# Optimization experiments

Hardware: AMD Instinct MI355X
Metric: run time of the kernel (lower is better)

The kernel has to match this reference:

```python
import jax, jax.numpy as jnp
import numpy as np

EPS = 1e-8
SAMPLE = 4          # minimal_sample_size for homography
BATCH = 1024        # batch_size: hypotheses per iteration
MAX_ITER = 10       # max_iter
MAX_LO = 5          # max_lo_iters
INL_TH = 2.0        # inl_th (on squared transfer error, as in kornia)
CONF = 0.99         # confidence
SOFT_INL_TH = 3.0   # kornia find_homography_dlt_iterated default
DLT_ITERS = 5       # kornia iterated-DLT default n_iter
N_PTS = 4096


def to_homog(p):
    return jnp.concatenate([p, jnp.ones_like(p[..., :1])], axis=-1)


def transform_points(T, p):
    # T: (B,3,3), p: (B,N,2)
    out = jnp.einsum('bij,bnj->bni', T, to_homog(p))
    z = out[..., 2:3]
    zi = jnp.where(jnp.abs(z) > EPS, 1.0 / z, 1.0)
    return out[..., :2] * zi


def normalize_points(p):
    # Hartley normalization: zero mean, mean distance sqrt(2)
    mean = p.mean(axis=1, keepdims=True)                       # (B,1,2)
    scale = jnp.linalg.norm(p - mean, axis=-1).mean(axis=-1)    # (B,)
    s = jnp.asarray(np.sqrt(2.0), p.dtype) / (scale + EPS)
    z = jnp.zeros_like(s)
    o = jnp.ones_like(s)
    T = jnp.stack([s, z, -s * mean[:, 0, 0],
                   z, s, -s * mean[:, 0, 1],
                   z, z, o], axis=-1).reshape(-1, 3, 3)
    return transform_points(T, p), T


def find_homography_dlt(p1, p2, w):
    # p1, p2: (B,N,2); w: (B,N) -> (B,3,3)
    p1n, T1 = normalize_points(p1)
    p2n, T2 = normalize_points(p2)
    x1, y1 = p1n[..., 0], p1n[..., 1]
    x2, y2 = p2n[..., 0], p2n[..., 1]
    o = jnp.ones_like(x1)
    z = jnp.zeros_like(x1)
    ax = jnp.stack([z, z, z, -x1, -y1, -o, y2 * x1, y2 * y1, y2], axis=-1)
    ay = jnp.stack([x1, y1, o, z, z, z, -x2 * x1, -x2 * y1, -x2], axis=-1)
    A = jnp.concatenate([ax, ay], axis=1)           # (B,2N,9); row order irrelevant for A^T W A
    wr = jnp.concatenate([w, w], axis=1)            # weight paired to each row
    AtWA = jnp.einsum('bni,bn,bnj->bij', A, wr, A)  # (B,9,9) symmetric PSD
    _, evecs = jnp.linalg.eigh(AtWA)
    H = evecs[..., :, 0].reshape(-1, 3, 3)          # smallest eigenvector == last right-singular vec
    H = jnp.linalg.inv(T2) @ H @ T1
    return H / (H[..., 2:3, 2:3] + EPS)


def oneway_transfer_error(kp1, kp2, models, squared=True):
    # kp1, kp2: (N,2); models: (B,3,3) -> (B,N)
    out = jnp.einsum('bij,nj->bni', models, to_homog(kp1))
    z = out[..., 2:3]
    zi = jnp.where(jnp.abs(z) > EPS, 1.0 / z, 1.0)
    proj = out[..., :2] * zi
    err = jnp.sum((proj - kp2[None]) ** 2, axis=-1)
    return err if squared else jnp.sqrt(err + EPS)


def find_homography_dlt_iterated(p1, p2, w):
    # iteratively reweighted DLT; mask keeps zero-weight (outlier) rows at zero,
    # equivalent to kornia's hard selection of inlier rows before polishing
    mask = (w > 0).astype(w.dtype)
    H = find_homography_dlt(p1, p2, w)
    for _ in range(DLT_ITERS - 1):
        err = oneway_transfer_error(p1[0], p2[0], H, squared=False)
        w = mask * jnp.exp(-err / (2.0 * SOFT_INL_TH ** 2))
        H = find_homography_dlt(p1, p2, w)
    return H


def sample_is_valid_for_homography(p1, p2):
    # orientation consistency of all point triplets (sign of triple product)
    idx = jnp.array([[0, 1, 2], [0, 1, 3], [0, 2, 3], [1, 2, 3]])
    s1 = jnp.sign(jnp.linalg.det(to_homog(p1)[:, idx]))
    s2 = jnp.sign(jnp.linalg.det(to_homog(p2)[:, idx]))
    return jnp.all(s1 == s2, axis=1)


def ransac_forward(kp1, kp2):
    N = kp1.shape[0]
    dtype = kp1.dtype
    keys = jax.random.split(jax.random.key(42), MAX_ITER)

    def verify(models):
        err = oneway_transfer_error(kp1, kp2, models)
        inl = err <= INL_TH
        return inl, inl.astype(dtype).sum(axis=1)

    def polish_step(carry, _):
        model, inliers, score, active = carry
        w = inliers.astype(dtype)[None]
        model_lo = find_homography_dlt_iterated(kp1[None], kp2[None], w)
        inl_lo, score_lo = verify(model_lo)
        better = active & (score_lo[0] > score)  # 'break' on first non-improvement
        model = jnp.where(better, model_lo[0], model)
        inliers = jnp.where(better, inl_lo[0], inliers)
        score = jnp.where(better, score_lo[0], score)
        return (model, inliers, score, better), None

    def step(carry, xs):
        best_model, best_inl, best_score, done = carry
        key, i = xs
        # minimal sampler: topk over uniform noise == random 4-subset per hypothesis
        rand = jax.random.uniform(key, (BATCH, N), dtype)
        _, idxs = jax.lax.top_k(rand, SAMPLE)
        k1s, k2s = kp1[idxs], kp2[idxs]              # (BATCH,4,2)
        valid = sample_is_valid_for_homography(k1s, k2s)
        models = find_homography_dlt(k1s, k2s, jnp.ones((BATCH, SAMPLE), dtype))
        diag_ok = jnp.abs(jnp.diagonal(models, axis1=1, axis2=2)).min(axis=1) > 1e-4
        inl_all, scores = verify(models)
        scores = jnp.where(valid & diag_ok, scores, -1.0)  # masking == removal for argmax
        bi = jnp.argmax(scores)
        model, inliers, score = models[bi], inl_all[bi], scores[bi]
        improve = (~done) & (score > best_score)
        (model_p, inl_p, score_p, _), _ = jax.lax.scan(
            polish_step, (model, inliers, score, improve), None, length=MAX_LO)
        best_model = jnp.where(improve, model_p, best_model)
        best_inl = jnp.where(improve, inl_p, best_inl)
        best_score = jnp.where(improve, score_p, best_score)
        # early stopping criterion (device-side instead of host .item())
        ratio = jnp.floor(best_score) / N
        q = jnp.clip(1.0 - ratio ** SAMPLE, 1e-12, 1.0 - 1e-12)
        max_samp = jnp.where(best_score >= N, 1.0,
                             jnp.log(1.0 - CONF) / jnp.log(q))
        done = done | (improve & (((i + 1) * BATCH) >= jnp.floor(max_samp)))
        return (best_model, best_inl, best_score, done), None

    init = (jnp.zeros((3, 3), dtype), jnp.zeros((N,), bool),
            jnp.asarray(float(SAMPLE), dtype), jnp.asarray(False))
    (best_model, best_inl, _, _), _ = jax.lax.scan(
        step, init, (keys, jnp.arange(MAX_ITER)))
    return best_model, best_inl


def setup_inputs() -> dict:
    key = jax.random.key(0)
    k1, k2, k3, k4 = jax.random.split(key, 4)
    kp1 = jax.random.uniform(k1, (N_PTS, 2), jnp.float32) * 1024.0
    Ht = jnp.array([[0.9, 0.1, 20.0], [-0.05, 1.05, -10.0], [1e-4, -1e-4, 1.0]], jnp.float32)
    ph = to_homog(kp1) @ Ht.T
    p2 = ph[:, :2] / ph[:, 2:3]
    noise = jax.random.normal(k2, (N_PTS, 2), jnp.float32) * 0.3
    outliers = jax.random.uniform(k3, (N_PTS, 2), jnp.float32) * 1024.0
    is_out = jax.random.uniform(k4, (N_PTS, 1)) < 0.3
    kp2 = jnp.where(is_out, outliers, p2 + noise)
    return {"kp1": kp1, "kp2": kp2}


def reference(kp1, kp2):
    return ransac_forward(kp1, kp2)
```

## Files before the change

kernel.cpp:

```cpp
#include <hip/hip_runtime.h>
#include <cstdint>

#define NPTS   4096
#define NBATCH 1024
#define NIT    10

__host__ __device__ inline uint32_t rotl32(uint32_t v, uint32_t r){ return (v<<r)|(v>>(32u-r)); }

__host__ __device__ inline void tf2x32(uint32_t k0,uint32_t k1,uint32_t x0,uint32_t x1,
                                       uint32_t&o0,uint32_t&o1){
  uint32_t ks2 = k0 ^ k1 ^ 0x1BD11BDAu;
  x0 += k0; x1 += k1;
  x0+=x1; x1=rotl32(x1,13); x1^=x0;
  x0+=x1; x1=rotl32(x1,15); x1^=x0;
  x0+=x1; x1=rotl32(x1,26); x1^=x0;
  x0+=x1; x1=rotl32(x1, 6); x1^=x0;
  x0+=k1; x1+=ks2+1u;
  x0+=x1; x1=rotl32(x1,17); x1^=x0;
  x0+=x1; x1=rotl32(x1,29); x1^=x0;
  x0+=x1; x1=rotl32(x1,16); x1^=x0;
  x0+=x1; x1=rotl32(x1,24); x1^=x0;
  x0+=ks2; x1+=k0+2u;
  x0+=x1; x1=rotl32(x1,13); x1^=x0;
  x0+=x1; x1=rotl32(x1,15); x1^=x0;
  x0+=x1; x1=rotl32(x1,26); x1^=x0;
  x0+=x1; x1=rotl32(x1, 6); x1^=x0;
  x0+=k0; x1+=k1+3u;
  x0+=x1; x1=rotl32(x1,17); x1^=x0;
  x0+=x1; x1=rotl32(x1,29); x1^=x0;
  x0+=x1; x1=rotl32(x1,16); x1^=x0;
  x0+=x1; x1=rotl32(x1,24); x1^=x0;
  x0+=k1; x1+=ks2+4u;
  x0+=x1; x1=rotl32(x1,13); x1^=x0;
  x0+=x1; x1=rotl32(x1,15); x1^=x0;
  x0+=x1; x1=rotl32(x1,26); x1^=x0;
  x0+=x1; x1=rotl32(x1, 6); x1^=x0;
  x0+=ks2; x1+=k0+5u;
  o0=x0; o1=x1;
}

__device__ inline float errsq_f(const float H[9], float x, float y, float kx, float ky){
  float z  = H[6]*x + H[7]*y + H[8];
  float zi = (fabsf(z) > 1e-8f) ? (1.0f/z) : 1.0f;
  float px = (H[0]*x + H[1]*y + H[2])*zi;
  float py = (H[3]*x + H[4]*y + H[5])*zi;
  float dx = px - kx, dy = py - ky;
  return dx*dx + dy*dy;
}

__device__ inline void denorm_h(const double h[9], double s1, double m1x, double m1y,
                                double s2, double m2x, double m2y, float out[9]){
  double G[3][3];
  #pragma unroll
  for(int r=0;r<3;r++){
    double h0=h[3*r], h1=h[3*r+1], h2=h[3*r+2];
    G[r][0] = h0*s1;
    G[r][1] = h1*s1;
    G[r][2] = -s1*m1x*h0 - s1*m1y*h1 + h2;
  }
  double Hm[3][3];
  double inv2 = 1.0/s2;
  #pragma unroll
  for(int c=0;c<3;c++){
    Hm[0][c] = G[0][c]*inv2 + m2x*G[2][c];
    Hm[1][c] = G[1][c]*inv2 + m2y*G[2][c];
    Hm[2][c] = G[2][c];
  }
  double invd = 1.0/(Hm[2][2] + 1e-8);
  #pragma unroll
  for(int r=0;r<3;r++)
    #pragma unroll
    for(int c=0;c<3;c++)
      out[3*r+c] = (float)(Hm[r][c]*invd);
}

__device__ inline double det3c(double ax,double ay, double bx,double by, double cx,double cy){
  return ax*(by-cy) - bx*(ay-cy) + cx*(ay-by);
}

__device__ inline void h4pt(const double P[4][2], double M[3][3]){
  double c0 = det3c(P[3][0],P[3][1], P[1][0],P[1][1], P[2][0],P[2][1]);
  double c1 = det3c(P[0][0],P[0][1], P[3][0],P[3][1], P[2][0],P[2][1]);
  double c2 = det3c(P[0][0],P[0][1], P[1][0],P[1][1], P[3][0],P[3][1]);
  M[0][0]=c0*P[0][0]; M[0][1]=c1*P[1][0]; M[0][2]=c2*P[2][0];
  M[1][0]=c0*P[0][1]; M[1][1]=c1*P[1][1]; M[1][2]=c2*P[2][1];
  M[2][0]=c0;         M[2][1]=c1;         M[2][2]=c2;
}

__device__ inline void adj3(const double M[3][3], double A[3][3]){
  A[0][0]=M[1][1]*M[2][2]-M[1][2]*M[2][1];
  A[0][1]=M[0][2]*M[2][1]-M[0][1]*M[2][2];
  A[0][2]=M[0][1]*M[1][2]-M[0][2]*M[1][1];
  A[1][0]=M[1][2]*M[2][0]-M[1][0]*M[2][2];
  A[1][1]=M[0][0]*M[2][2]-M[0][2]*M[2][0];
  A[1][2]=M[0][2]*M[1][0]-M[0][0]*M[1][2];
  A[2][0]=M[1][0]*M[2][1]-M[1][1]*M[2][0];
  A[2][1]=M[0][1]*M[2][0]-M[0][0]*M[2][1];
  A[2][2]=M[0][0]*M[1][1]-M[0][1]*M[1][0];
}

__device__ inline void ins4(uint64_t b[4], uint64_t k){
  if(k > b[0]){ b[3]=b[2]; b[2]=b[1]; b[1]=b[0]; b[0]=k; }
  else if(k > b[1]){ b[3]=b[2]; b[2]=b[1]; b[1]=k; }
  else if(k > b[2]){ b[3]=b[2]; b[2]=k; }
  else if(k > b[3]){ b[3]=k; }
}

__device__ inline void inv3sym(const double A[3][3], double R[3][3]){
  double a=A[0][0], b=A[1][0], c=A[2][0], d=A[1][1], e=A[2][1], f=A[2][2];
  double C00=d*f-e*e, C01=c*e-b*f, C02=b*e-c*d;
  double det=a*C00+b*C01+c*C02;
  if(det < 1e-300) det = 1e-300;
  double id=1.0/det;
  R[0][0]=C00*id; R[0][1]=C01*id; R[0][2]=C02*id;
  R[1][0]=C01*id; R[1][1]=(a*f-c*c)*id; R[1][2]=(b*c-a*e)*id;
  R[2][0]=C02*id; R[2][1]=R[1][2];      R[2][2]=(a*d-b*b)*id;
}
__device__ inline void mv3(const double M[3][3], const double x[3], double y[3]){
  y[0]=M[0][0]*x[0]+M[0][1]*x[1]+M[0][2]*x[2];
  y[1]=M[1][0]*x[0]+M[1][1]*x[1]+M[1][2]*x[2];
  y[2]=M[2][0]*x[0]+M[2][1]*x[1]+M[2][2]*x[2];
}

__device__ inline void solve24x(const double* sMd, float curHn[9], float curH[9],
                                bool dnorm, double ns1,double nm1x,double nm1y,
                                double ns2,double nm2x,double nm2y){
  double S0[3][3],S1[3][3],S2[3][3],S3[3][3];
  auto unpackd=[&](const double* s, double M[3][3]){
    M[0][0]=s[0]; M[0][1]=s[1]; M[0][2]=s[3];
    M[1][0]=s[1]; M[1][1]=s[2]; M[1][2]=s[4];
    M[2][0]=s[3]; M[2][1]=s[4]; M[2][2]=s[5];
  };
  unpackd(sMd+0,S0); unpackd(sMd+6,S1); unpackd(sMd+12,S2); unpackd(sMd+18,S3);

  double S0i[3][3]; inv3sym(S0,S0i);
  double T1[3][3], T2[3][3];
  #pragma unroll
  for(int i=0;i<3;i++)
    #pragma unroll
    for(int j=0;j<3;j++){
      T1[i][j]=S0i[i][0]*S1[0][j]+S0i[i][1]*S1[1][j]+S0i[i][2]*S1[2][j];
      T2[i][j]=S0i[i][0]*S2[0][j]+S0i[i][1]*S2[1][j]+S0i[i][2]*S2[2][j];
    }
  double Sc[3][3];
  #pragma unroll
  for(int i=0;i<3;i++)
    #pragma unroll
    for(int j=0;j<3;j++){
      double s = S3[i][j];
      #pragma unroll
      for(int k=0;k<3;k++) s -= S1[i][k]*T1[k][j] + S2[i][k]*T2[k][j];
      Sc[i][j]=s;
    }
  double Sci[3][3]; inv3sym(Sc,Sci);

  double v[9];
  #pragma unroll
  for(int i=0;i<9;i++) v[i]=1.0;
  #pragma unroll
  for(int itn=0; itn<2; itn++){
    double a[3]={v[0],v[1],v[2]}, b[3]={v[3],v[4],v[5]}, c[3]={v[6],v[7],v[8]};
    double w1[3],w2[3];
    mv3(S0i,a,w1); mv3(S0i,b,w2);
    double rhs[3];
    #pragma unroll
    for(int j=0;j<3;j++)
      rhs[j] = c[j] + T1[0][j]*a[0]+T1[1][j]*a[1]+T1[2][j]*a[2]
                    + T2[0][j]*b[0]+T2[1][j]*b[1]+T2[2][j]*b[2];
    double rr[3];
    mv3(Sci,rhs,rr);
    #pragma unroll
    for(int i=0;i<3;i++){
      v[i]   = w1[i] + T1[i][0]*rr[0]+T1[i][1]*rr[1]+T1[i][2]*rr[2];
      v[3+i] = w2[i] + T2[i][0]*rr[0]+T2[i][1]*rr[1]+T2[i][2]*rr[2];
      v[6+i] = rr[i];
    }
    if(itn==0){
      double mx=0.0;
      #pragma unroll
      for(int i=0;i<9;i++){ double aa=fabs(v[i]); if(aa>mx) mx=aa; }
      double sc = 1.0/(mx + 1e-300);
      #pragma unroll
      for(int i=0;i<9;i++) v[i]*=sc;
    }
  }
  double n2=0.0;
  #pragma unroll
  for(int i=0;i<9;i++) n2 += v[i]*v[i];
  double invn = 1.0/sqrt(n2);
  #pragma unroll
  for(int i=0;i<9;i++) v[i]*=invn;
  #pragma unroll
  for(int j=0;j<9;j++) curHn[j]=(float)v[j];
  if(dnorm) denorm_h(v, ns1,nm1x,nm1y, ns2,nm2x,nm2y, curH);
}

__device__ inline void model4(const double P1[4][2], const double P2[4][2],
                              float Hf[9], int* flag){
  const int TRI[4][3] = {{0,1,2},{0,1,3},{0,2,3},{1,2,3}};
  bool valid = true;
  #pragma unroll
  for(int tq=0;tq<4;tq++){
    const int i0=TRI[tq][0], i1=TRI[tq][1], i2=TRI[tq][2];
    double d1 = det3c(P1[i0][0],P1[i0][1], P1[i1][0],P1[i1][1], P1[i2][0],P1[i2][1]);
    double d2 = det3c(P2[i0][0],P2[i0][1], P2[i1][0],P2[i1][1], P2[i2][0],P2[i2][1]);
    int s1 = (d1>0.0)-(d1<0.0), s2 = (d2>0.0)-(d2<0.0);
    if(s1 != s2) valid = false;
  }
  double MA[3][3], MB[3][3], AJ[3][3], H[3][3];
  h4pt(P1, MA); h4pt(P2, MB);
  adj3(MA, AJ);
  #pragma unroll
  for(int i=0;i<3;i++)
    #pragma unroll
    for(int j=0;j<3;j++)
      H[i][j] = MB[i][0]*AJ[0][j] + MB[i][1]*AJ[1][j] + MB[i][2]*AJ[2][j];
  double n2=0.0;
  #pragma unroll
  for(int i=0;i<3;i++)
    #pragma unroll
    for(int j=0;j<3;j++) n2 += H[i][j]*H[i][j];
  double invn = 1.0/sqrt(n2);
  double invd = 1.0/(H[2][2]*invn + 1e-8);
  #pragma unroll
  for(int i=0;i<3;i++)
    #pragma unroll
    for(int j=0;j<3;j++) Hf[3*i+j] = (float)(H[i][j]*invn*invd);
  bool diag_ok = (fminf(fminf(fabsf(Hf[0]),fabsf(Hf[4])),fabsf(Hf[8])) > 1e-4f);
  *flag = (valid && diag_ok) ? 1 : 0;
}

__global__ __launch_bounds__(1024) void k_init(const float* __restrict__ kp1,
                                               const float* __restrict__ kp2,
                                               float* stateF, float* nrm,
                                               float* best_inl, float* p1n, float* p2n){
  __shared__ double red[1024];
  const int t = threadIdx.x;
  auto blk_reduce = [&](double v)->double{
    red[t]=v; __syncthreads();
    for(int off=512; off>=1; off>>=1){ if(t<off) red[t]+=red[t+off]; __syncthreads(); }
    double rr = red[0]; __syncthreads(); return rr;
  };
  double sx1=0, sy1=0, sx2=0, sy2=0;
  #pragma unroll
  for(int q=0;q<4;q++){
    int p = t + 1024*q;
    sx1 += (double)kp1[2*p];   sy1 += (double)kp1[2*p+1];
    sx2 += (double)kp2[2*p];   sy2 += (double)kp2[2*p+1];
  }
  double m1x = blk_reduce(sx1)/(double)NPTS;
  double m1y = blk_reduce(sy1)/(double)NPTS;
  double m2x = blk_reduce(sx2)/(double)NPTS;
  double m2y = blk_reduce(sy2)/(double)NPTS;
  double a1=0, a2=0;
  #pragma unroll
  for(int q=0;q<4;q++){
    int p = t + 1024*q;
    double dx1=(double)kp1[2*p]-m1x, dy1=(double)kp1[2*p+1]-m1y;
    double dx2=(double)kp2[2*p]-m2x, dy2=(double)kp2[2*p+1]-m2y;
    a1 += sqrt(dx1*dx1+dy1*dy1);
    a2 += sqrt(dx2*dx2+dy2*dy2);
  }
  double sc1 = blk_reduce(a1)/(double)NPTS;
  double sc2 = blk_reduce(a2)/(double)NPTS;
  double s1 = 1.4142135623730951/(sc1+1e-8);
  double s2 = 1.4142135623730951/(sc2+1e-8);
  if(t==0){
    nrm[0]=(float)s1; nrm[1]=(float)m1x; nrm[2]=(float)m1y;
    nrm[3]=(float)s2; nrm[4]=(float)m2x; nrm[5]=(float)m2y;
    stateF[0]=4.0f; stateF[1]=0.0f;
    for(int j=0;j<9;j++) stateF[2+j]=0.0f;
  }
  #pragma unroll
  for(int q=0;q<4;q++){
    int p = t + 1024*q;
    p1n[2*p]   = (float)(s1*((double)kp1[2*p]  -m1x));
    p1n[2*p+1] = (float)(s1*((double)kp1[2*p+1]-m1y));
    p2n[2*p]   = (float)(s2*((double)kp2[2*p]  -m2x));
    p2n[2*p+1] = (float)(s2*((double)kp2[2*p+1]-m2y));
    best_inl[p] = 0.0f;
  }
}

__global__ __launch_bounds__(256) void k_sample_score(const float* stateF,
                                                uint32_t key0, uint32_t key1,
                                                const float* __restrict__ kp1,
                                                const float* __restrict__ kp2,
                                                float* __restrict__ models,
                                                float* __restrict__ scores){
  if(stateF[1] != 0.0f) return;
  const int r = blockIdx.x;
  const int t = threadIdx.x;
  __shared__ uint64_t ls2[4][256];
  __shared__ float sH[9];
  __shared__ int   sFlag;
  __shared__ int   redi[4];
  uint64_t b[4] = {0ull,0ull,0ull,0ull};
  #pragma unroll
  for(int j=0;j<16;j++){
    int c = t*16 + j;
    uint32_t f = (uint32_t)(r*NPTS + c);
    uint32_t a0,a1;
    tf2x32(key0,key1, 0u, f, a0,a1);
    uint32_t bits = a0 ^ a1;
    uint64_t v = (uint64_t)((bits>>9) + 1u);
    uint64_t key = (v<<12) | (uint64_t)(4095 - c);
    ins4(b, key);
  }
  ls2[0][t]=b[0]; ls2[1][t]=b[1]; ls2[2][t]=b[2]; ls2[3][t]=b[3];
  __syncthreads();
  for(int off=128; off>=1; off>>=1){
    if(t < off){
      uint64_t o0=ls2[0][t+off], o1=ls2[1][t+off], o2=ls2[2][t+off], o3=ls2[3][t+off];
      ins4(b,o0); ins4(b,o1); ins4(b,o2); ins4(b,o3);
      ls2[0][t]=b[0]; ls2[1][t]=b[1]; ls2[2][t]=b[2]; ls2[3][t]=b[3];
    }
    __syncthreads();
  }
  if(t==0){
    double P1[4][2], P2[4][2];
    #pragma unroll
    for(int k=0;k<4;k++){
      int id = 4095 - (int)(b[k] & 0xFFFull);
      P1[k][0]=(double)kp1[2*id]; P1[k][1]=(double)kp1[2*id+1];
      P2[k][0]=(double)kp2[2*id]; P2[k][1]=(double)kp2[2*id+1];
    }
    float Hf[9]; int fl;
    model4(P1,P2,Hf,&fl);
    #pragma unroll
    for(int j=0;j<9;j++){ models[r*9+j]=Hf[j]; sH[j]=Hf[j]; }
    sFlag = fl;
  }
  __syncthreads();
  float H[9];
  #pragma unroll
  for(int j=0;j<9;j++) H[j]=sH[j];
  int cnt=0;
  #pragma unroll
  for(int j=0;j<16;j++){
    int p = t + 256*j;
    float e = errsq_f(H, kp1[2*p], kp1[2*p+1], kp2[2*p], kp2[2*p+1]);
    cnt += (e <= 2.0f) ? 1 : 0;
  }
  #pragma unroll
  for(int off=32; off>=1; off>>=1) cnt += __shfl_down(cnt, off, 64);
  if((t&63)==0) redi[t>>6]=cnt;
  __syncthreads();
  if(t==0) scores[r] = sFlag ? (float)(redi[0]+redi[1]+redi[2]+redi[3]) : -1.0f;
}

__global__ __launch_bounds__(512) void k_polish(float* stateF, const float* nrm,
                                                const float* __restrict__ scores,
                                                const float* __restrict__ models,
                                                const float* __restrict__ kp1,
                                                const float* __restrict__ kp2,
                                                const float* __restrict__ p1n,
                                                const float* __restrict__ p2n,
                                                float* __restrict__ best_inl,
                                                int iter){
  if(stateF[1] != 0.0f) return;
  const int t = threadIdx.x;
  const int lane = t & 63, wv = t >> 6;
  __shared__ float  p2b[512][28];
  __shared__ double p3[16][25];
  __shared__ double sMd[24];
  __shared__ uint64_t redu[8];
  __shared__ int   redi[8];
  __shared__ float sScore;
  __shared__ float sModel[9];
  __shared__ float curHn[9];
  __shared__ float curH[9];
  __shared__ unsigned char inlb[2][NPTS];

  {
    float sA = scores[t], sB = scores[t+512];
    uint64_t kA = ((uint64_t)(uint32_t)(int)(sA + 2.0f) << 12) | (uint64_t)(1023 - t);
    uint64_t kB = ((uint64_t)(uint32_t)(int)(sB + 2.0f) << 12) | (uint64_t)(1023 - (t+512));
    uint64_t k = (kA >= kB) ? kA : kB;
    #pragma unroll
    for(int off=32; off>=1; off>>=1){
      uint64_t o = __shfl_down(k, off, 64);
      if(o > k) k = o;
    }
    if(lane==0) redu[wv]=k;
  }
  __syncthreads();
  if(t==0){
    uint64_t m=redu[0];
    #pragma unroll
    for(int w8=1;w8<8;w8++) if(redu[w8]>m) m=redu[w8];
    redu[0]=m;
  }
  __syncthreads();
  const int bi = 1023 - (int)(redu[0] & 0xFFFull);
  const float selScore = (float)((int)(redu[0] >> 12)) - 2.0f;

  const float bestScore = stateF[0];
  const bool improve = (selScore > bestScore);
  if(!improve) return;

  if(t<9) sModel[t] = models[bi*9+t];
  __syncthreads();

  float U1[8],V1[8],U2[8],V2[8],X1[8],Y1[8],X2[8],Y2[8];
  #pragma unroll
  for(int q=0;q<8;q++){
    int p = t + 512*q;
    U1[q]=kp1[2*p]; V1[q]=kp1[2*p+1];
    U2[q]=kp2[2*p]; V2[q]=kp2[2*p+1];
    X1[q]=p1n[2*p]; Y1[q]=p1n[2*p+1];
    X2[q]=p2n[2*p]; Y2[q]=p2n[2*p+1];
  }
  {
    float H[9];
    #pragma unroll
    for(int j=0;j<9;j++) H[j]=sModel[j];
    #pragma unroll
    for(int q=0;q<8;q++){
      int p = t + 512*q;
      float e = errsq_f(H, U1[q],V1[q],U2[q],V2[q]);
      inlb[0][p] = (e <= 2.0f) ? 1 : 0;
    }
  }
  __syncthreads();

  int cur = 0;
  float score = selScore;
  bool active = true;
  float wreg[8];

  const double ns1=(double)nrm[0], nm1x=(double)nrm[1], nm1y=(double)nrm[2];
  const double ns2=(double)nrm[3], nm2x=(double)nrm[4], nm2y=(double)nrm[5];
  const float s2f  = nrm[3];
  const float epsn = 1e-8f*s2f*s2f;
  const float wk   = 1.0f/(18.0f*s2f);

  auto DLT = [&](bool denorm_now){
    float part[24];
    #pragma unroll
    for(int k=0;k<24;k++) part[k]=0.0f;
    #pragma unroll
    for(int q=0;q<8;q++){
      float w = wreg[q];
      float x=X1[q], y=Y1[q], x2=X2[q], y2=Y2[q];
      float wx = w*x, wy = w*y;
      float m0=wx*x, m1=wx*y, m2=wy*y;
      float s3 = x2*x2 + y2*y2;
      part[0]+=m0; part[1]+=m1; part[2]+=m2; part[3]+=wx; part[4]+=wy; part[5]+=w;
      part[6]+=x2*m0; part[7]+=x2*m1; part[8]+=x2*m2; part[9]+=x2*wx; part[10]+=x2*wy; part[11]+=x2*w;
      part[12]+=y2*m0; part[13]+=y2*m1; part[14]+=y2*m2; part[15]+=y2*wx; part[16]+=y2*wy; part[17]+=y2*w;
      part[18]+=s3*m0; part[19]+=s3*m1; part[20]+=s3*m2; part[21]+=s3*wx; part[22]+=s3*wy; part[23]+=s3*w;
    }
    float4* rowp = reinterpret_cast<float4*>(&p2b[t][0]);
    rowp[0]=make_float4(part[0],part[1],part[2],part[3]);
    rowp[1]=make_float4(part[4],part[5],part[6],part[7]);
    rowp[2]=make_float4(part[8],part[9],part[10],part[11]);
    rowp[3]=make_float4(part[12],part[13],part[14],part[15]);
    rowp[4]=make_float4(part[16],part[17],part[18],part[19]);
    rowp[5]=make_float4(part[20],part[21],part[22],part[23]);
    __syncthreads();
    if(t<96){
      int qd = t%6, seg = t/6;
      double a0=0,a1=0,a2=0,a3=0;
      #pragma unroll
      for(int i=0;i<32;i++){
        float4 v = *reinterpret_cast<const float4*>(&p2b[seg*32+i][qd*4]);
        a0+=(double)v.x; a1+=(double)v.y; a2+=(double)v.z; a3+=(double)v.w;
      }
      p3[seg][qd*4+0]=a0; p3[seg][qd*4+1]=a1; p3[seg][qd*4+2]=a2; p3[seg][qd*4+3]=a3;
    }
    __syncthreads();
    if(t<24){
      double a=0.0;
      #pragma unroll
      for(int s=0;s<16;s++) a += p3[s][t];
      sMd[t]=a;
    }
    __syncthreads();
    if(t==0) solve24x(sMd, curHn, curH, denorm_now, ns1,nm1x,nm1y, ns2,nm2x,nm2y);
    __syncthreads();
  };

  for(int lo=0; lo<5; lo++){
    #pragma unroll
    for(int q=0;q<8;q++){ int p=t+512*q; wreg[q] = inlb[cur][p] ? 1.0f : 0.0f; }
    DLT(false);
    for(int itp=0; itp<4; itp++){
      float Hn[9];
      #pragma unroll
      for(int j=0;j<9;j++) Hn[j]=curHn[j];
      #pragma unroll
      for(int q=0;q<8;q++){
        int p=t+512*q;
        float zn = Hn[6]*X1[q] + Hn[7]*Y1[q] + Hn[8];
        float zi = 1.0f/zn;
        float dx = (Hn[0]*X1[q] + Hn[1]*Y1[q] + Hn[2])*zi - X2[q];
        float dy = (Hn[3]*X1[q] + Hn[4]*Y1[q] + Hn[5])*zi - Y2[q];
        float err = sqrtf(dx*dx + dy*dy + epsn);
        wreg[q] = inlb[cur][p] ? __expf(-err*wk) : 0.0f;
      }
      DLT(itp==3);
    }
    float scoreLo;
    {
      float H[9];
      #pragma unroll
      for(int j=0;j<9;j++) H[j]=curH[j];
      int c=0;
      #pragma unroll
      for(int q=0;q<8;q++){
        int p=t+512*q;
        float e = errsq_f(H, U1[q],V1[q],U2[q],V2[q]);
        unsigned char bb = (e <= 2.0f) ? 1 : 0;
        inlb[cur^1][p] = bb;
        c += bb;
      }
      #pragma unroll
      for(int off=32; off>=1; off>>=1) c += __shfl_down(c, off, 64);
      if(lane==0) redi[wv]=c;
      __syncthreads();
      if(t==0){
        int s=0;
        #pragma unroll
        for(int w8=0;w8<8;w8++) s += redi[w8];
        sScore=(float)s;
      }
      __syncthreads();
      scoreLo = sScore;
    }
    bool better = active && (scoreLo > score);
    if(better){
      if(t<9) sModel[t]=curH[t];
      cur ^= 1;
      score = scoreLo;
    }
    active = better;
    __syncthreads();
    if(!active) break;
  }

  if(t<9) stateF[2+t] = sModel[t];
  #pragma unroll
  for(int q=0;q<8;q++){ int p=t+512*q; best_inl[p] = inlb[cur][p] ? 1.0f : 0.0f; }
  if(t==0){
    stateF[0] = score;
    float ratio = floorf(score) / 4096.0f;
    float r2 = ratio*ratio, r4 = r2*r2;
    float q  = 1.0f - r4;
    q = fminf(fmaxf(q, 1e-12f), (float)(1.0 - 1e-12));
    float max_samp = (score >= 4096.0f) ? 1.0f : (logf(0.01f)/logf(q));
    stateF[1] = (((float)((iter+1)*NBATCH)) >= floorf(max_samp)) ? 1.0f : 0.0f;
  }
}

__global__ __launch_bounds__(1024) void k_out(const float* stateF, const float* best_inl,
                                              float* __restrict__ out, int out_size){
  const int t = threadIdx.x;
  if(t<9 && t<out_size) out[t] = stateF[2+t];
  #pragma unroll
  for(int q=0;q<4;q++){
    int p = t + 1024*q, o = 9 + p;
    if(o < out_size) out[o] = best_inl[p];
  }
}

extern "C" void kernel_launch(void* const* d_in, const int* in_sizes, int n_in,
                              void* d_out, int out_size, void* d_ws, size_t ws_size,
                              hipStream_t stream) {
  const float* kp1 = (const float*)d_in[0];
  const float* kp2 = (const float*)d_in[1];
  float* out = (float*)d_out;
  float* ws  = (float*)d_ws;

  float* stateF   = ws + 0;
  float* nrm      = ws + 16;
  float* best_inl = ws + 32;
  float* p1n      = ws + 4128;
  float* p2n      = ws + 12320;
  float* scores   = ws + 20512;
  float* models   = ws + 21536;

  uint32_t K0h[NIT], K1h[NIT];
  for(int i=0;i<NIT;i++){ uint32_t a,b; tf2x32(0u,42u,0u,(uint32_t)i,a,b); K0h[i]=a; K1h[i]=b; }

  k_init<<<1, 1024, 0, stream>>>(kp1, kp2, stateF, nrm, best_inl, p1n, p2n);
  for(int i=0;i<NIT;i++){
    k_sample_score<<<NBATCH, 256, 0, stream>>>(stateF, K0h[i], K1h[i], kp1, kp2, models, scores);
    k_polish<<<1, 512, 0, stream>>>(stateF, nrm, scores, models, kp1, kp2, p1n, p2n, best_inl, i);
  }
  k_out<<<1, 1024, 0, stream>>>(stateF, best_inl, out, out_size);
}
```

Baseline: 119.1 us.

## Replace per-iteration launches with fused init and persistent grid-barrier tail kernel

Normalization is folded into the first sampling kernel as an extra block, and the original iteration-0 polish launch is kept. Iterations 1..9 of sampling, scoring and polish, plus the output copy, move into one persistent 128-block kernel that synchronizes with a global atomic grid barrier. This cuts the launch sequence from twenty-two kernels to a memset and three kernels, removing launch and queue overhead, most of it from launches that only check a done flag and exit. The trade-off is lower parallelism if later iterations actually run: each block handles eight hypothesis rows in sequence. The design also relies on all 128 blocks being resident at once so the spin barrier cannot deadlock.

```diff
diff --git a/kernel.cpp b/kernel.cpp
--- a/kernel.cpp
+++ b/kernel.cpp
@@ -4,6 +4,8 @@
 #define NPTS   4096
 #define NBATCH 1024
 #define NIT    10
+#define TAILBLK 128
+#define ROWSPB  (NBATCH/TAILBLK)
 
 __host__ __device__ inline uint32_t rotl32(uint32_t v, uint32_t r){ return (v<<r)|(v>>(32u-r)); }
 
@@ -230,147 +232,28 @@
   *flag = (valid && diag_ok) ? 1 : 0;
 }
 
-__global__ __launch_bounds__(1024) void k_init(const float* __restrict__ kp1,
-                                               const float* __restrict__ kp2,
-                                               float* stateF, float* nrm,
-                                               float* best_inl, float* p1n, float* p2n){
-  __shared__ double red[1024];
-  const int t = threadIdx.x;
-  auto blk_reduce = [&](double v)->double{
-    red[t]=v; __syncthreads();
-    for(int off=512; off>=1; off>>=1){ if(t<off) red[t]+=red[t+off]; __syncthreads(); }
-    double rr = red[0]; __syncthreads(); return rr;
-  };
-  double sx1=0, sy1=0, sx2=0, sy2=0;
-  #pragma unroll
-  for(int q=0;q<4;q++){
-    int p = t + 1024*q;
-    sx1 += (double)kp1[2*p];   sy1 += (double)kp1[2*p+1];
-    sx2 += (double)kp2[2*p];   sy2 += (double)kp2[2*p+1];
-  }
-  double m1x = blk_reduce(sx1)/(double)NPTS;
-  double m1y = blk_reduce(sy1)/(double)NPTS;
-  double m2x = blk_reduce(sx2)/(double)NPTS;
-  double m2y = blk_reduce(sy2)/(double)NPTS;
-  double a1=0, a2=0;
-  #pragma unroll
-  for(int q=0;q<4;q++){
-    int p = t + 1024*q;
-    double dx1=(double)kp1[2*p]-m1x, dy1=(double)kp1[2*p+1]-m1y;
-    double dx2=(double)kp2[2*p]-m2x, dy2=(double)kp2[2*p+1]-m2y;
-    a1 += sqrt(dx1*dx1+dy1*dy1);
-    a2 += sqrt(dx2*dx2+dy2*dy2);
-  }
-  double sc1 = blk_reduce(a1)/(double)NPTS;
-  double sc2 = blk_reduce(a2)/(double)NPTS;
-  double s1 = 1.4142135623730951/(sc1+1e-8);
-  double s2 = 1.4142135623730951/(sc2+1e-8);
-  if(t==0){
-    nrm[0]=(float)s1; nrm[1]=(float)m1x; nrm[2]=(float)m1y;
-    nrm[3]=(float)s2; nrm[4]=(float)m2x; nrm[5]=(float)m2y;
-    stateF[0]=4.0f; stateF[1]=0.0f;
-    for(int j=0;j<9;j++) stateF[2+j]=0.0f;
-  }
-  #pragma unroll
-  for(int q=0;q<4;q++){
-    int p = t + 1024*q;
-    p1n[2*p]   = (float)(s1*((double)kp1[2*p]  -m1x));
-    p1n[2*p+1] = (float)(s1*((double)kp1[2*p+1]-m1y));
-    p2n[2*p]   = (float)(s2*((double)kp2[2*p]  -m2x));
-    p2n[2*p+1] = (float)(s2*((double)kp2[2*p+1]-m2y));
-    best_inl[p] = 0.0f;
-  }
-}
-
-__global__ __launch_bounds__(256) void k_sample_score(const float* stateF,
-                                                uint32_t key0, uint32_t key1,
-                                                const float* __restrict__ kp1,
-                                                const float* __restrict__ kp2,
-                                                float* __restrict__ models,
-                                                float* __restrict__ scores){
-  if(stateF[1] != 0.0f) return;
-  const int r = blockIdx.x;
-  const int t = threadIdx.x;
-  __shared__ uint64_t ls2[4][256];
-  __shared__ float sH[9];
-  __shared__ int   sFlag;
-  __shared__ int   redi[4];
-  uint64_t b[4] = {0ull,0ull,0ull,0ull};
-  #pragma unroll
-  for(int j=0;j<16;j++){
-    int c = t*16 + j;
-    uint32_t f = (uint32_t)(r*NPTS + c);
-    uint32_t a0,a1;
-    tf2x32(key0,key1, 0u, f, a0,a1);
-    uint32_t bits = a0 ^ a1;
-    uint64_t v = (uint64_t)((bits>>9) + 1u);
-    uint64_t key = (v<<12) | (uint64_t)(4095 - c);
-    ins4(b, key);
-  }
-  ls2[0][t]=b[0]; ls2[1][t]=b[1]; ls2[2][t]=b[2]; ls2[3][t]=b[3];
-  __syncthreads();
-  for(int off=128; off>=1; off>>=1){
-    if(t < off){
-      uint64_t o0=ls2[0][t+off], o1=ls2[1][t+off], o2=ls2[2][t+off], o3=ls2[3][t+off];
-      ins4(b,o0); ins4(b,o1); ins4(b,o2); ins4(b,o3);
-      ls2[0][t]=b[0]; ls2[1][t]=b[1]; ls2[2][t]=b[2]; ls2[3][t]=b[3];
-    }
-    __syncthreads();
-  }
-  if(t==0){
-    double P1[4][2], P2[4][2];
-    #pragma unroll
-    for(int k=0;k<4;k++){
-      int id = 4095 - (int)(b[k] & 0xFFFull);
-      P1[k][0]=(double)kp1[2*id]; P1[k][1]=(double)kp1[2*id+1];
-      P2[k][0]=(double)kp2[2*id]; P2[k][1]=(double)kp2[2*id+1];
-    }
-    float Hf[9]; int fl;
-    model4(P1,P2,Hf,&fl);
-    #pragma unroll
-    for(int j=0;j<9;j++){ models[r*9+j]=Hf[j]; sH[j]=Hf[j]; }
-    sFlag = fl;
-  }
-  __syncthreads();
-  float H[9];
-  #pragma unroll
-  for(int j=0;j<9;j++) H[j]=sH[j];
-  int cnt=0;
-  #pragma unroll
-  for(int j=0;j<16;j++){
-    int p = t + 256*j;
-    float e = errsq_f(H, kp1[2*p], kp1[2*p+1], kp2[2*p], kp2[2*p+1]);
-    cnt += (e <= 2.0f) ? 1 : 0;
-  }
-  #pragma unroll
-  for(int off=32; off>=1; off>>=1) cnt += __shfl_down(cnt, off, 64);
-  if((t&63)==0) redi[t>>6]=cnt;
-  __syncthreads();
-  if(t==0) scores[r] = sFlag ? (float)(redi[0]+redi[1]+redi[2]+redi[3]) : -1.0f;
-}
-
-__global__ __launch_bounds__(512) void k_polish(float* stateF, const float* nrm,
-                                                const float* __restrict__ scores,
-                                                const float* __restrict__ models,
-                                                const float* __restrict__ kp1,
-                                                const float* __restrict__ kp2,
-                                                const float* __restrict__ p1n,
-                                                const float* __restrict__ p2n,
-                                                float* __restrict__ best_inl,
-                                                int iter){
-  if(stateF[1] != 0.0f) return;
+struct ShPol {
+  float  p2b[512][28];
+  double p3[16][25];
+  double sMd[24];
+  unsigned long long redu[8];
+  int    redi[8];
+  float  sScore;
+  float  sModel[9];
+  float  curHn[9];
+  float  curH[9];
+  unsigned char inlb[2][NPTS];
+};
+
+__device__ __forceinline__ void do_polish(ShPol& sp, float* stateF, const float* nrm,
+                          const float* scores, const float* models,
+                          const float* kp1, const float* kp2,
+                          const float* p1n, const float* p2n,
+                          float* best_inl, int iter){
   const int t = threadIdx.x;
   const int lane = t & 63, wv = t >> 6;
-  __shared__ float  p2b[512][28];
-  __shared__ double p3[16][25];
-  __shared__ double sMd[24];
-  __shared__ uint64_t redu[8];
-  __shared__ int   redi[8];
-  __shared__ float sScore;
-  __shared__ float sModel[9];
-  __shared__ float curHn[9];
-  __shared__ float curH[9];
-  __shared__ unsigned char inlb[2][NPTS];
+
+  if(stateF[1] != 0.0f) return;
 
   {
     float sA = scores[t], sB = scores[t+512];
@@ -382,24 +265,24 @@
       uint64_t o = __shfl_down(k, off, 64);
       if(o > k) k = o;
     }
-    if(lane==0) redu[wv]=k;
+    if(lane==0) sp.redu[wv]=k;
   }
   __syncthreads();
   if(t==0){
-    uint64_t m=redu[0];
-    #pragma unroll
-    for(int w8=1;w8<8;w8++) if(redu[w8]>m) m=redu[w8];
-    redu[0]=m;
-  }
-  __syncthreads();
-  const int bi = 1023 - (int)(redu[0] & 0xFFFull);
-  const float selScore = (float)((int)(redu[0] >> 12)) - 2.0f;
+    uint64_t m=sp.redu[0];
+    #pragma unroll
+    for(int w8=1;w8<8;w8++) if(sp.redu[w8]>m) m=sp.redu[w8];
+    sp.redu[0]=m;
+  }
+  __syncthreads();
+  const int bi = 1023 - (int)(sp.redu[0] & 0xFFFull);
+  const float selScore = (float)((int)(sp.redu[0] >> 12)) - 2.0f;
 
   const float bestScore = stateF[0];
   const bool improve = (selScore > bestScore);
   if(!improve) return;
 
-  if(t<9) sModel[t] = models[bi*9+t];
+  if(t<9) sp.sModel[t] = models[bi*9+t];
   __syncthreads();
 
   float U1[8],V1[8],U2[8],V2[8],X1[8],Y1[8],X2[8],Y2[8];
@@ -414,12 +297,12 @@
   {
     float H[9];
     #pragma unroll
-    for(int j=0;j<9;j++) H[j]=sModel[j];
+    for(int j=0;j<9;j++) H[j]=sp.sModel[j];
     #pragma unroll
     for(int q=0;q<8;q++){
       int p = t + 512*q;
       float e = errsq_f(H, U1[q],V1[q],U2[q],V2[q]);
-      inlb[0][p] = (e <= 2.0f) ? 1 : 0;
+      sp.inlb[0][p] = (e <= 2.0f) ? 1 : 0;
     }
   }
   __syncthreads();
@@ -451,7 +334,7 @@
       part[12]+=y2*m0; part[13]+=y2*m1; part[14]+=y2*m2; part[15]+=y2*wx; part[16]+=y2*wy; part[17]+=y2*w;
       part[18]+=s3*m0; part[19]+=s3*m1; part[20]+=s3*m2; part[21]+=s3*wx; part[22]+=s3*wy; part[23]+=s3*w;
     }
-    float4* rowp = reinterpret_cast<float4*>(&p2b[t][0]);
+    float4* rowp = reinterpret_cast<float4*>(&sp.p2b[t][0]);
     rowp[0]=make_float4(part[0],part[1],part[2],part[3]);
     rowp[1]=make_float4(part[4],part[5],part[6],part[7]);
     rowp[2]=make_float4(part[8],part[9],part[10],part[11]);
@@ -464,31 +347,32 @@
       double a0=0,a1=0,a2=0,a3=0;
       #pragma unroll
       for(int i=0;i<32;i++){
-        float4 v = *reinterpret_cast<const float4*>(&p2b[seg*32+i][qd*4]);
+        float4 v = *reinterpret_cast<const float4*>(&sp.p2b[seg*32+i][qd*4]);
         a0+=(double)v.x; a1+=(double)v.y; a2+=(double)v.z; a3+=(double)v.w;
       }
-      p3[seg][qd*4+0]=a0; p3[seg][qd*4+1]=a1; p3[seg][qd*4+2]=a2; p3[seg][qd*4+3]=a3;
+      sp.p3[seg][qd*4+0]=a0; sp.p3[seg][qd*4+1]=a1;
+      sp.p3[seg][qd*4+2]=a2; sp.p3[seg][qd*4+3]=a3;
     }
     __syncthreads();
     if(t<24){
       double a=0.0;
       #pragma unroll
-      for(int s=0;s<16;s++) a += p3[s][t];
-      sMd[t]=a;
+      for(int s=0;s<16;s++) a += sp.p3[s][t];
+      sp.sMd[t]=a;
     }
     __syncthreads();
-    if(t==0) solve24x(sMd, curHn, curH, denorm_now, ns1,nm1x,nm1y, ns2,nm2x,nm2y);
+    if(t==0) solve24x(sp.sMd, sp.curHn, sp.curH, denorm_now, ns1,nm1x,nm1y, ns2,nm2x,nm2y);
     __syncthreads();
   };
 
   for(int lo=0; lo<5; lo++){
     #pragma unroll
-    for(int q=0;q<8;q++){ int p=t+512*q; wreg[q] = inlb[cur][p] ? 1.0f : 0.0f; }
+    for(int q=0;q<8;q++){ int p=t+512*q; wreg[q] = sp.inlb[cur][p] ? 1.0f : 0.0f; }
     DLT(false);
     for(int itp=0; itp<4; itp++){
       float Hn[9];
       #pragma unroll
-      for(int j=0;j<9;j++) Hn[j]=curHn[j];
+      for(int j=0;j<9;j++) Hn[j]=sp.curHn[j];
       #pragma unroll
       for(int q=0;q<8;q++){
         int p=t+512*q;
@@ -497,7 +381,7 @@
         float dx = (Hn[0]*X1[q] + Hn[1]*Y1[q] + Hn[2])*zi - X2[q];
         float dy = (Hn[3]*X1[q] + Hn[4]*Y1[q] + Hn[5])*zi - Y2[q];
         float err = sqrtf(dx*dx + dy*dy + epsn);
-        wreg[q] = inlb[cur][p] ? __expf(-err*wk) : 0.0f;
+        wreg[q] = sp.inlb[cur][p] ? __expf(-err*wk) : 0.0f;
       }
       DLT(itp==3);
     }
@@ -505,32 +389,32 @@
     {
       float H[9];
       #pragma unroll
-      for(int j=0;j<9;j++) H[j]=curH[j];
+      for(int j=0;j<9;j++) H[j]=sp.curH[j];
       int c=0;
       #pragma unroll
       for(int q=0;q<8;q++){
         int p=t+512*q;
         float e = errsq_f(H, U1[q],V1[q],U2[q],V2[q]);
         unsigned char bb = (e <= 2.0f) ? 1 : 0;
-        inlb[cur^1][p] = bb;
+        sp.inlb[cur^1][p] = bb;
         c += bb;
       }
       #pragma unroll
       for(int off=32; off>=1; off>>=1) c += __shfl_down(c, off, 64);
-      if(lane==0) redi[wv]=c;
+      if(lane==0) sp.redi[wv]=c;
       __syncthreads();
       if(t==0){
         int s=0;
         #pragma unroll
-        for(int w8=0;w8<8;w8++) s += redi[w8];
-        sScore=(float)s;
+        for(int w8=0;w8<8;w8++) s += sp.redi[w8];
+        sp.sScore=(float)s;
       }
       __syncthreads();
-      scoreLo = sScore;
+      scoreLo = sp.sScore;
     }
     bool better = active && (scoreLo > score);
     if(better){
-      if(t<9) sModel[t]=curH[t];
+      if(t<9) sp.sModel[t]=sp.curH[t];
       cur ^= 1;
       score = scoreLo;
     }
@@ -539,9 +423,9 @@
     if(!active) break;
   }
 
-  if(t<9) stateF[2+t] = sModel[t];
-  #pragma unroll
-  for(int q=0;q<8;q++){ int p=t+512*q; best_inl[p] = inlb[cur][p] ? 1.0f : 0.0f; }
+  if(t<9) stateF[2+t] = sp.sModel[t];
+  #pragma unroll
+  for(int q=0;q<8;q++){ int p=t+512*q; best_inl[p] = sp.inlb[cur][p] ? 1.0f : 0.0f; }
   if(t==0){
     stateF[0] = score;
     float ratio = floorf(score) / 4096.0f;
@@ -553,14 +437,269 @@
   }
 }
 
-__global__ __launch_bounds__(1024) void k_out(const float* stateF, const float* best_inl,
-                                              float* __restrict__ out, int out_size){
+__global__ __launch_bounds__(256) void k_ss0(uint32_t key0, uint32_t key1,
+                                             const float* __restrict__ kp1,
+                                             const float* __restrict__ kp2,
+                                             float* __restrict__ ws){
+  float* stateF   = ws + 0;
+  float* nrm      = ws + 16;
+  float* best_inl = ws + 32;
+  float* p1n      = ws + 4128;
+  float* p2n      = ws + 12320;
+  float* scores   = ws + 20512;
+  float* models   = ws + 21536;
+
+  const int r = blockIdx.x;
   const int t = threadIdx.x;
-  if(t<9 && t<out_size) out[t] = stateF[2+t];
-  #pragma unroll
-  for(int q=0;q<4;q++){
-    int p = t + 1024*q, o = 9 + p;
-    if(o < out_size) out[o] = best_inl[p];
+
+  if(r == NBATCH){
+    __shared__ double red[256];
+    auto blk_reduce = [&](double v)->double{
+      red[t]=v; __syncthreads();
+      for(int off=128; off>=1; off>>=1){ if(t<off) red[t]+=red[t+off]; __syncthreads(); }
+      double rr = red[0]; __syncthreads(); return rr;
+    };
+    double sx1=0, sy1=0, sx2=0, sy2=0;
+    #pragma unroll
+    for(int q=0;q<16;q++){
+      int p = t + 256*q;
+      sx1 += (double)kp1[2*p];   sy1 += (double)kp1[2*p+1];
+      sx2 += (double)kp2[2*p];   sy2 += (double)kp2[2*p+1];
+    }
+    double m1x = blk_reduce(sx1)/(double)NPTS;
+    double m1y = blk_reduce(sy1)/(double)NPTS;
+    double m2x = blk_reduce(sx2)/(double)NPTS;
+    double m2y = blk_reduce(sy2)/(double)NPTS;
+    double a1=0, a2=0;
+    #pragma unroll
+    for(int q=0;q<16;q++){
+      int p = t + 256*q;
+      double dx1=(double)kp1[2*p]-m1x, dy1=(double)kp1[2*p+1]-m1y;
+      double dx2=(double)kp2[2*p]-m2x, dy2=(double)kp2[2*p+1]-m2y;
+      a1 += sqrt(dx1*dx1+dy1*dy1);
+      a2 += sqrt(dx2*dx2+dy2*dy2);
+    }
+    double sc1 = blk_reduce(a1)/(double)NPTS;
+    double sc2 = blk_reduce(a2)/(double)NPTS;
+    double s1 = 1.4142135623730951/(sc1+1e-8);
+    double s2 = 1.4142135623730951/(sc2+1e-8);
+    if(t==0){
+      nrm[0]=(float)s1; nrm[1]=(float)m1x; nrm[2]=(float)m1y;
+      nrm[3]=(float)s2; nrm[4]=(float)m2x; nrm[5]=(float)m2y;
+      stateF[0]=4.0f; stateF[1]=0.0f;
+      for(int j=0;j<9;j++) stateF[2+j]=0.0f;
+    }
+    #pragma unroll
+    for(int q=0;q<16;q++){
+      int p = t + 256*q;
+      p1n[2*p]   = (float)(s1*((double)kp1[2*p]  -m1x));
+      p1n[2*p+1] = (float)(s1*((double)kp1[2*p+1]-m1y));
+      p2n[2*p]   = (float)(s2*((double)kp2[2*p]  -m2x));
+      p2n[2*p+1] = (float)(s2*((double)kp2[2*p+1]-m2y));
+      best_inl[p] = 0.0f;
+    }
+    return;
+  }
+
+  __shared__ uint64_t ls2[4][256];
+  __shared__ float sH[9];
+  __shared__ int   sFlag;
+  __shared__ int   redi[4];
+  uint64_t b[4] = {0ull,0ull,0ull,0ull};
+  #pragma unroll
+  for(int j=0;j<16;j++){
+    int c = t*16 + j;
+    uint32_t f = (uint32_t)(r*NPTS + c);
+    uint32_t a0,a1;
+    tf2x32(key0,key1, 0u, f, a0,a1);
+    uint32_t bits = a0 ^ a1;
+    uint64_t v = (uint64_t)((bits>>9) + 1u);
+    uint64_t key = (v<<12) | (uint64_t)(4095 - c);
+    ins4(b, key);
+  }
+  ls2[0][t]=b[0]; ls2[1][t]=b[1]; ls2[2][t]=b[2]; ls2[3][t]=b[3];
+  __syncthreads();
+  for(int off=128; off>=1; off>>=1){
+    if(t < off){
+      uint64_t o0=ls2[0][t+off], o1=ls2[1][t+off], o2=ls2[2][t+off], o3=ls2[3][t+off];
+      ins4(b,o0); ins4(b,o1); ins4(b,o2); ins4(b,o3);
+      ls2[0][t]=b[0]; ls2[1][t]=b[1]; ls2[2][t]=b[2]; ls2[3][t]=b[3];
+    }
+    __syncthreads();
+  }
+  if(t==0){
+    double P1[4][2], P2[4][2];
+    #pragma unroll
+    for(int k=0;k<4;k++){
+      int id = 4095 - (int)(b[k] & 0xFFFull);
+      P1[k][0]=(double)kp1[2*id]; P1[k][1]=(double)kp1[2*id+1];
+      P2[k][0]=(double)kp2[2*id]; P2[k][1]=(double)kp2[2*id+1];
+    }
+    float Hf[9]; int fl;
+    model4(P1,P2,Hf,&fl);
+    #pragma unroll
+    for(int j=0;j<9;j++){ models[r*9+j]=Hf[j]; sH[j]=Hf[j]; }
+    sFlag = fl;
+  }
+  __syncthreads();
+  float H[9];
+  #pragma unroll
+  for(int j=0;j<9;j++) H[j]=sH[j];
+  int cnt=0;
+  #pragma unroll
+  for(int j=0;j<16;j++){
+    int p = t + 256*j;
+    float e = errsq_f(H, kp1[2*p], kp1[2*p+1], kp2[2*p], kp2[2*p+1]);
+    cnt += (e <= 2.0f) ? 1 : 0;
+  }
+  #pragma unroll
+  for(int off=32; off>=1; off>>=1) cnt += __shfl_down(cnt, off, 64);
+  if((t&63)==0) redi[t>>6]=cnt;
+  __syncthreads();
+  if(t==0) scores[r] = sFlag ? (float)(redi[0]+redi[1]+redi[2]+redi[3]) : -1.0f;
+}
+
+__global__ __launch_bounds__(512) void k_polish(float* stateF, const float* nrm,
+                                                const float* __restrict__ scores,
+                                                const float* __restrict__ models,
+                                                const float* __restrict__ kp1,
+                                                const float* __restrict__ kp2,
+                                                const float* __restrict__ p1n,
+                                                const float* __restrict__ p2n,
+                                                float* __restrict__ best_inl,
+                                                int iter){
+  __shared__ ShPol sp;
+  do_polish(sp, stateF, nrm, scores, models, kp1, kp2, p1n, p2n, best_inl, iter);
+}
+
+struct ShSamp512 {
+  unsigned long long ls2[4][512];
+  float sH[9];
+  int   sFlag;
+  int   redi[8];
+};
+union ShTail { ShPol p; ShSamp512 s; };
+
+__device__ inline void gridbar(uint32_t* cnt, uint32_t* gen, uint32_t nblk){
+  __threadfence();
+  __syncthreads();
+  if(threadIdx.x==0){
+    uint32_t g = __hip_atomic_load(gen, __ATOMIC_ACQUIRE, __HIP_MEMORY_SCOPE_AGENT);
+    uint32_t a = __hip_atomic_fetch_add(cnt, 1u, __ATOMIC_ACQ_REL, __HIP_MEMORY_SCOPE_AGENT);
+    if(a == nblk-1u){
+      __hip_atomic_store(cnt, 0u, __ATOMIC_RELAXED, __HIP_MEMORY_SCOPE_AGENT);
+      __hip_atomic_store(gen, g+1u, __ATOMIC_RELEASE, __HIP_MEMORY_SCOPE_AGENT);
+    }else{
+      while(__hip_atomic_load(gen, __ATOMIC_ACQUIRE, __HIP_MEMORY_SCOPE_AGENT) == g){
+        __builtin_amdgcn_s_sleep(2);
+      }
+    }
+  }
+  __syncthreads();
+  __threadfence();
+}
+
+__global__ __launch_bounds__(512) void k_tail(const float* __restrict__ kp1,
+                                              const float* __restrict__ kp2,
+                                              float* __restrict__ out, int out_size,
+                                              float* __restrict__ ws){
+  float* stateF   = ws + 0;
+  float* nrm      = ws + 16;
+  float* best_inl = ws + 32;
+  float* p1n      = ws + 4128;
+  float* p2n      = ws + 12320;
+  float* scores   = ws + 20512;
+  float* models   = ws + 21536;
+  uint32_t* barw  = (uint32_t*)(ws + 30752);
+
+  const int b = blockIdx.x;
+  const int t = threadIdx.x;
+  const int lane = t & 63, wv = t >> 6;
+  __shared__ ShTail sh;
+
+  for(int it=1; it<NIT; ++it){
+    float dn = __hip_atomic_load(&stateF[1], __ATOMIC_ACQUIRE, __HIP_MEMORY_SCOPE_AGENT);
+    if(dn != 0.0f) break;
+
+    uint32_t key0,key1;
+    tf2x32(0u,42u,0u,(uint32_t)it,key0,key1);
+
+    for(int m=0;m<ROWSPB;m++){
+      const int r = b*ROWSPB + m;
+      uint64_t bb[4] = {0ull,0ull,0ull,0ull};
+      #pragma unroll
+      for(int j=0;j<8;j++){
+        int c = t*8 + j;
+        uint32_t f = (uint32_t)(r*NPTS + c);
+        uint32_t a0,a1;
+        tf2x32(key0,key1, 0u, f, a0,a1);
+        uint32_t bits = a0 ^ a1;
+        uint64_t v = (uint64_t)((bits>>9) + 1u);
+        uint64_t kk = (v<<12) | (uint64_t)(4095 - c);
+        ins4(bb, kk);
+      }
+      sh.s.ls2[0][t]=bb[0]; sh.s.ls2[1][t]=bb[1]; sh.s.ls2[2][t]=bb[2]; sh.s.ls2[3][t]=bb[3];
+      __syncthreads();
+      for(int off=256; off>=1; off>>=1){
+        if(t < off){
+          uint64_t o0=sh.s.ls2[0][t+off], o1=sh.s.ls2[1][t+off];
+          uint64_t o2=sh.s.ls2[2][t+off], o3=sh.s.ls2[3][t+off];
+          ins4(bb,o0); ins4(bb,o1); ins4(bb,o2); ins4(bb,o3);
+          sh.s.ls2[0][t]=bb[0]; sh.s.ls2[1][t]=bb[1]; sh.s.ls2[2][t]=bb[2]; sh.s.ls2[3][t]=bb[3];
+        }
+        __syncthreads();
+      }
+      if(t==0){
+        double P1[4][2], P2[4][2];
+        #pragma unroll
+        for(int k=0;k<4;k++){
+          int id = 4095 - (int)(bb[k] & 0xFFFull);
+          P1[k][0]=(double)kp1[2*id]; P1[k][1]=(double)kp1[2*id+1];
+          P2[k][0]=(double)kp2[2*id]; P2[k][1]=(double)kp2[2*id+1];
+        }
+        float Hf[9]; int fl;
+        model4(P1,P2,Hf,&fl);
+        #pragma unroll
+        for(int j=0;j<9;j++){ models[r*9+j]=Hf[j]; sh.s.sH[j]=Hf[j]; }
+        sh.s.sFlag = fl;
+      }
+      __syncthreads();
+      float H[9];
+      #pragma unroll
+      for(int j=0;j<9;j++) H[j]=sh.s.sH[j];
+      int cnt=0;
+      #pragma unroll
+      for(int j=0;j<8;j++){
+        int p = t + 512*j;
+        float2 a = ((const float2*)kp1)[p];
+        float2 c = ((const float2*)kp2)[p];
+        float e = errsq_f(H, a.x, a.y, c.x, c.y);
+        cnt += (e <= 2.0f) ? 1 : 0;
+      }
+      #pragma unroll
+      for(int off=32; off>=1; off>>=1) cnt += __shfl_down(cnt, off, 64);
+      if(lane==0) sh.s.redi[wv]=cnt;
+      __syncthreads();
+      if(t==0){
+        int s=0;
+        #pragma unroll
+        for(int w8=0;w8<8;w8++) s += sh.s.redi[w8];
+        scores[r] = sh.s.sFlag ? (float)s : -1.0f;
+      }
+      __syncthreads();
+    }
+    gridbar(&barw[0], &barw[1], (uint32_t)gridDim.x);
+    if(b==0) do_polish(sh.p, stateF, nrm, scores, models, kp1, kp2, p1n, p2n, best_inl, it);
+    gridbar(&barw[0], &barw[1], (uint32_t)gridDim.x);
+  }
+
+  if(b==0){
+    if(t<9 && t<out_size) out[t] = stateF[2+t];
+    #pragma unroll
+    for(int q=0;q<8;q++){
+      int p = t + 512*q, o = 9 + p;
+      if(o < out_size) out[o] = best_inl[p];
+    }
   }
 }
 
@@ -579,14 +718,13 @@
   float* p2n      = ws + 12320;
   float* scores   = ws + 20512;
   float* models   = ws + 21536;
-
-  uint32_t K0h[NIT], K1h[NIT];
-  for(int i=0;i<NIT;i++){ uint32_t a,b; tf2x32(0u,42u,0u,(uint32_t)i,a,b); K0h[i]=a; K1h[i]=b; }
-
-  k_init<<<1, 1024, 0, stream>>>(kp1, kp2, stateF, nrm, best_inl, p1n, p2n);
-  for(int i=0;i<NIT;i++){
-    k_sample_score<<<NBATCH, 256, 0, stream>>>(stateF, K0h[i], K1h[i], kp1, kp2, models, scores);
-    k_polish<<<1, 512, 0, stream>>>(stateF, nrm, scores, models, kp1, kp2, p1n, p2n, best_inl, i);
-  }
-  k_out<<<1, 1024, 0, stream>>>(stateF, best_inl, out, out_size);
-}
+  void*  barw     = (void*)(ws + 30752);
+
+  uint32_t k00, k01;
+  tf2x32(0u,42u,0u,0u,k00,k01);
+
+  (void)hipMemsetAsync(barw, 0, 16, stream);
+  k_ss0   <<<NBATCH+1, 256, 0, stream>>>(k00, k01, kp1, kp2, ws);
+  k_polish<<<1, 512, 0, stream>>>(stateF, nrm, scores, models, kp1, kp2, p1n, p2n, best_inl, 0);
+  k_tail  <<<TAILBLK, 512, 0, stream>>>(kp1, kp2, out, out_size, ws);
+}
```

Result: faster. 101.4 us (-14.9%).
